# Optimization experiments

Measured on AMD Instinct MI355X. Metric: run time of the kernel, lower is better.

The kernel has to match this reference:

```python
import jax, jax.numpy as jnp
import numpy as np
from jax.scipy.special import gammaln, xlogy

B, S, C = 2, 2048, 1536
H, DK, DV = 8, 64, 192
F_REL = C // H  # 192 relative-position features


def positional_features_all(positions, feature_size, seq_length):
    # positions: [1, 2S-1] float32 (signed relative distances)
    n = feature_size // 6  # basis per class per sign
    ap = jnp.abs(positions)  # [1, 2S-1]
    Sf = float(seq_length)
    # exponential decay features
    max_range = float(np.log(Sf) / np.log(2.0))
    half_life = 2.0 ** jnp.linspace(3.0, max_range, n)  # min_half_life = 3.0
    feat_exp = jnp.exp(-jnp.log(2.0) / half_life * ap[..., None])
    # central mask features
    center_widths = 2.0 ** jnp.arange(1, n + 1, dtype=jnp.float32) - 1.0
    feat_cm = (center_widths > ap[..., None]).astype(jnp.float32)
    # gamma pdf features
    stddev = Sf / (2.0 * n)
    start_mean = Sf / n
    mean = jnp.linspace(start_mean, Sf, n)
    conc = (mean / stddev) ** 2
    rate = mean / (stddev ** 2)
    xg = ap[..., None]
    log_unnorm = xlogy(conc - 1.0, xg) - rate * xg
    log_norm = gammaln(conc) - conc * jnp.log(rate)
    prob = jnp.exp(log_unnorm - log_norm) + 1e-8
    feat_g = prob / jnp.max(prob, axis=1, keepdims=True)
    emb = jnp.concatenate([feat_exp, feat_cm, feat_g], axis=-1)  # [1, 2S-1, 3n]
    emb = jnp.concatenate([emb, jnp.sign(positions)[..., None] * emb], axis=-1)
    return emb  # [1, 2S-1, feature_size]


def relative_shift(x):
    # x: [B, H, T, 2T-1] -> [B, H, T, T] (Transformer-XL shift trick)
    b, h, t, _ = x.shape
    x = jnp.pad(x, ((0, 0), (0, 0), (0, 0), (1, 0)))  # [B,H,T,2T]
    x = x.reshape(b, h, 2 * t, t)[:, :, 1:, :]          # [B,H,2T-1,T]
    x = x.reshape(b, h, t, 2 * t - 1)[:, :, :, :t]      # [B,H,T,T]
    return x


def setup_inputs() -> dict:
    key = jax.random.key(0)
    ks = jax.random.split(key, 8)
    inp = {
        "x": jax.random.normal(ks[0], (B, S, C), dtype=jnp.float32),
        "mask": jax.random.randint(ks[1], (B, S), 0, 2, dtype=jnp.int32),
        "Wq": jax.random.normal(ks[2], (C, H * DK), dtype=jnp.float32) * 0.02,
        "Wk": jax.random.normal(ks[3], (C, H * DK), dtype=jnp.float32) * 0.02,
        "Wv": jax.random.normal(ks[4], (C, H * DV), dtype=jnp.float32) * 0.02,
        "Wr": jax.random.normal(ks[5], (F_REL, H * DK), dtype=jnp.float32) * 0.02,
        "r_w_bias": jax.random.normal(ks[6], (1, H, 1, DK), dtype=jnp.float32) * 0.02,
        "Wo": jax.random.normal(ks[7], (H * DV, H * DV), dtype=jnp.float32) * 0.02,
        "bo": jnp.zeros((H * DV,), dtype=jnp.float32),
    }
    return inp


def reference(x, mask, Wq, Wk, Wv, Wr, r_w_bias, Wo, bo):
    b, s, c = x.shape
    # projections -> [B, H, S, d]
    q = (x @ Wq).reshape(b, s, H, DK).transpose(0, 2, 1, 3) * (DK ** -0.5)
    k = (x @ Wk).reshape(b, s, H, DK).transpose(0, 2, 1, 3)
    v = (x @ Wv).reshape(b, s, H, DV).transpose(0, 2, 1, 3)
    # relative positional encodings for distances -S+1 .. S-1
    dist = jnp.arange(-s + 1, s, dtype=jnp.float32)[None, :]  # [1, 2S-1]
    pe = positional_features_all(dist, F_REL, s)               # [1, 2S-1, F_REL]
    r_k = (pe[0] @ Wr).reshape(2 * s - 1, H, DK).transpose(1, 0, 2)  # [H, 2S-1, DK]
    # content + position logits
    content_logits = jnp.einsum('bhqd,bhkd->bhqk', q, k)                   # [B,H,S,S]
    rel_logits = jnp.einsum('bhqd,hkd->bhqk', q + r_w_bias, r_k)           # [B,H,S,2S-1]
    logits = content_logits + relative_shift(rel_logits)
    logits = jnp.where(mask[:, None, None, :] == 0, -1e9, logits)
    weights = jax.nn.softmax(logits, axis=-1)
    out = jnp.einsum('bhqk,bhkd->bhqd', weights, v)  # [B,H,S,DV]
    out = out.transpose(0, 2, 1, 3).reshape(b, s, H * DV)
    return out @ Wo + bo
```

## Files before the change

### kernel.cpp

```cpp
#include <hip/hip_runtime.h>
#include <math.h>

#define SEQ 2048
#define CDIM 1536
#define HN 8
#define DVC 192
#define BN 2
#define NPOS 4095
#define HDK 512
#define HDV 1536
#define PSTR 72

typedef __attribute__((ext_vector_type(8))) _Float16 hf8v;
typedef __attribute__((ext_vector_type(4))) _Float16 hf4v;
typedef __attribute__((ext_vector_type(4))) float f4v;

static __device__ __forceinline__ f4v mfma16(hf8v a, hf8v b, f4v c) {
  return __builtin_amdgcn_mfma_f32_16x16x32_f16(a, b, c, 0, 0, 0);
}
static __device__ __forceinline__ void gl2lds16(const void* g, void* l) {
  __builtin_amdgcn_global_load_lds((const __attribute__((address_space(1))) unsigned int*)g,
                                   (__attribute__((address_space(3))) unsigned int*)l,
                                   16, 0, 0);
}
static __device__ __forceinline__ float rowmax16(float x) {
  x = fmaxf(x, __int_as_float(__builtin_amdgcn_update_dpp(0, __float_as_int(x), 0x128, 0xf, 0xf, true)));
  x = fmaxf(x, __int_as_float(__builtin_amdgcn_update_dpp(0, __float_as_int(x), 0x124, 0xf, 0xf, true)));
  x = fmaxf(x, __int_as_float(__builtin_amdgcn_update_dpp(0, __float_as_int(x), 0x122, 0xf, 0xf, true)));
  x = fmaxf(x, __int_as_float(__builtin_amdgcn_update_dpp(0, __float_as_int(x), 0x121, 0xf, 0xf, true)));
  return x;
}

#define CAST_B 6144
#define TWQ_B  768
#define TWK_B  768
#define TWV_B  2304
#define TWO_B  2304
#define TWR_B  96
#define PE_B   1536
#define TW_END (CAST_B + TWQ_B + TWK_B + TWV_B + TWO_B + TWR_B)
#define PREP_BLOCKS (TW_END + PE_B)

__device__ __forceinline__ void twc_tile(const float* __restrict__ W, _Float16* __restrict__ WT,
                                         int K, int N, int tile, float (*tls)[33], int tid) {
  int ntn = N >> 5;
  int nt = tile % ntn, kt = tile / ntn;
  int k0 = kt * 32, n0 = nt * 32;
  int tx = tid & 31, ty = tid >> 5;
#pragma unroll
  for (int p = 0; p < 4; p++) tls[ty + p * 8][tx] = W[(size_t)(k0 + ty + p * 8) * N + n0 + tx];
  __syncthreads();
#pragma unroll
  for (int p = 0; p < 4; p++) {
    int n = ty + p * 8;
    WT[(size_t)(n0 + n) * K + k0 + tx] = (_Float16)tls[tx][n];
  }
}

__global__ __launch_bounds__(256) void prep_kernel(
    const float* __restrict__ x, const float* __restrict__ Wq, const float* __restrict__ Wk,
    const float* __restrict__ Wv, const float* __restrict__ Wo, const float* __restrict__ Wr,
    _Float16* __restrict__ xb, _Float16* __restrict__ WTqkv, _Float16* __restrict__ WoT,
    _Float16* __restrict__ WrT, _Float16* __restrict__ pe_h) {
  __shared__ float tls[32][33];
  int blk = blockIdx.x, tid = threadIdx.x;
  if (blk < CAST_B) {
    int i = (blk * 256 + tid) * 4;
    float4 v = *(const float4*)(x + i);
    _Float16 o[4] = {(_Float16)v.x, (_Float16)v.y, (_Float16)v.z, (_Float16)v.w};
    *(unsigned long long*)(xb + i) = *(const unsigned long long*)o;
  } else if (blk < CAST_B + TWQ_B) {
    twc_tile(Wq, WTqkv + 0 * (size_t)CDIM, CDIM, HDK, blk - CAST_B, tls, tid);
  } else if (blk < CAST_B + TWQ_B + TWK_B) {
    twc_tile(Wk, WTqkv + 512 * (size_t)CDIM, CDIM, HDK, blk - (CAST_B + TWQ_B), tls, tid);
  } else if (blk < CAST_B + TWQ_B + TWK_B + TWV_B) {
    twc_tile(Wv, WTqkv + 1024 * (size_t)CDIM, CDIM, HDV, blk - (CAST_B + TWQ_B + TWK_B), tls, tid);
  } else if (blk < CAST_B + TWQ_B + TWK_B + TWV_B + TWO_B) {
    twc_tile(Wo, WoT, CDIM, HDV, blk - (CAST_B + TWQ_B + TWK_B + TWV_B), tls, tid);
  } else if (blk < TW_END) {
    twc_tile(Wr, WrT, 192, HDK, blk - (CAST_B + TWQ_B + TWK_B + TWV_B + TWO_B), tls, tid);
  } else {
    int idx = (blk - TW_END) * 256 + tid;
    int pos = idx / 96, f = idx - pos * 96;
    float val = 0.0f, sval = 0.0f;
    if (pos < NPOS) {
      float ap = fabsf((float)(pos - (SEQ - 1)));
      int j = f & 31, cls = f >> 5;
      if (cls == 0) {
        float hl = exp2f(3.0f + 8.0f * (float)j / 31.0f);
        val = exp2f(-ap / hl);
      } else if (cls == 1) {
        float cw = exp2f((float)(j + 1)) - 1.0f;
        val = (cw > ap) ? 1.0f : 0.0f;
      } else {
        float conc = 4.0f * (float)((j + 1) * (j + 1));
        float rate = (float)(j + 1) / 16.0f;
        float log_norm = lgammaf(conc) - conc * logf(rate);
        float pv = expf((conc - 1.0f) * logf(ap) - rate * ap - log_norm) + 1e-8f;
        float mode = (conc - 1.0f) / rate;
        float a0 = fminf(floorf(mode), 2047.0f);
        float a1 = fminf(a0 + 1.0f, 2047.0f);
        float p0 = expf((conc - 1.0f) * logf(a0) - rate * a0 - log_norm) + 1e-8f;
        float p1 = expf((conc - 1.0f) * logf(a1) - rate * a1 - log_norm) + 1e-8f;
        val = pv / fmaxf(p0, p1);
      }
      float sgn = (pos > SEQ - 1) ? 1.0f : ((pos < SEQ - 1) ? -1.0f : 0.0f);
      sval = sgn * val;
    }
    pe_h[pos * 192 + f] = (_Float16)val;
    pe_h[pos * 192 + 96 + f] = (_Float16)sval;
  }
}

__global__ __launch_bounds__(256, 3) void mfma_gemm_qkvrk(
    const _Float16* __restrict__ xb, const _Float16* __restrict__ WTqkv,
    const _Float16* __restrict__ pe_h, const _Float16* __restrict__ WrT,
    _Float16* __restrict__ qb, _Float16* __restrict__ kb, _Float16* __restrict__ vtb,
    _Float16* __restrict__ rkb) {
  __shared__ __align__(16) _Float16 As[128 * 64];
  __shared__ __align__(16) _Float16 Bs[128 * 64];
  const int tid = threadIdx.x;
  const int lane = tid & 63, l15 = lane & 15, quad = lane >> 4;
  const int wv = tid >> 6;
  const int wm = (wv & 1) * 64, wn = (wv >> 1) * 64;
  const bool isrk = blockIdx.x >= 640;
  const _Float16* A;
  const _Float16* B;
  int K, ntx, lin, cpx;
  if (!isrk) {
    A = xb; B = WTqkv; K = CDIM; ntx = 20; lin = blockIdx.x; cpx = 80;
  } else {
    A = pe_h; B = WrT; K = 192; ntx = 4; lin = blockIdx.x - 640; cpx = 16;
  }
  const int sw = (lin & 7) * cpx + (lin >> 3);
  const int row0 = (sw / ntx) * 128, col0 = (sw % ntx) * 128;
  f4v acc[4][4];
#pragma unroll
  for (int i = 0; i < 4; i++)
#pragma unroll
    for (int j = 0; j < 4; j++) acc[i][j] = (f4v)0.0f;

  for (int k0 = 0; k0 < K; k0 += 64) {
    __syncthreads();
#pragma unroll
    for (int p = 0; p < 4; p++) {
      int idx = tid + p * 256;
      int rr = idx >> 3, sc = idx & 7;
      int gc = (sc ^ (rr & 7)) << 3;
      gl2lds16(A + (size_t)(row0 + rr) * K + k0 + gc, As + idx * 8);
      gl2lds16(B + (size_t)(col0 + rr) * K + k0 + gc, Bs + idx * 8);
    }
    __syncthreads();
#pragma unroll
    for (int kc = 0; kc < 2; kc++) {
      hf8v af[4], bfr[4];
#pragma unroll
      for (int t = 0; t < 4; t++) {
        int lrA = wm + t * 16 + l15;
        int lrB = wn + t * 16 + l15;
        af[t]  = *(const hf8v*)(As + lrA * 64 + ((((kc << 2) | quad) ^ (lrA & 7)) << 3));
        bfr[t] = *(const hf8v*)(Bs + lrB * 64 + ((((kc << 2) | quad) ^ (lrB & 7)) << 3));
      }
#pragma unroll
      for (int mt = 0; mt < 4; mt++)
#pragma unroll
        for (int nt = 0; nt < 4; nt++)
          acc[mt][nt] = mfma16(af[mt], bfr[nt], acc[mt][nt]);
    }
  }
#pragma unroll
  for (int mt = 0; mt < 4; mt++)
#pragma unroll
    for (int reg = 0; reg < 4; reg++) {
      int r = row0 + wm + mt * 16 + quad * 4 + reg;
      int bb = r >> 11, ss = r & (SEQ - 1);
#pragma unroll
      for (int nt = 0; nt < 4; nt++) {
        int c = col0 + wn + nt * 16 + l15;
        float vv = acc[mt][nt][reg];
        if (!isrk) {
          if (c < 512) {
            qb[(size_t)r * HDK + c] = (_Float16)(vv * 0.125f);
          } else if (c < 1024) {
            int cc = c - 512, h = cc >> 6, d = cc & 63;
            kb[(((size_t)bb * HN + h) * SEQ + ss) * 64 + d] = (_Float16)vv;
          } else {
            int cc = c - 1024, h = cc / DVC, e = cc - h * DVC;
            int jp = (ss & ~63) | ((ss & 15) << 2) | ((ss >> 4) & 3);
            vtb[(((size_t)bb * HN + h) * DVC + e) * SEQ + jp] = (_Float16)vv;
          }
        } else {
          int h = c >> 6, d = c & 63;
          rkb[((size_t)h * 4096 + r) * 64 + d] = (_Float16)vv;
        }
      }
    }
}

__global__ __launch_bounds__(256, 3) void mfma_gemm_out(
    const _Float16* __restrict__ A, const _Float16* __restrict__ B,
    const float* __restrict__ bias, float* __restrict__ out) {
  __shared__ __align__(16) _Float16 As[64 * 64];
  __shared__ __align__(16) _Float16 Bs[128 * 64];
  const int K = CDIM, ntx = 12;
  const int tid = threadIdx.x;
  const int lane = tid & 63, l15 = lane & 15, quad = lane >> 4;
  const int wv = tid >> 6;
  const int wm = (wv & 1) * 32, wn = (wv >> 1) * 64;
  const int lin = blockIdx.x;
  const int cpx = gridDim.x >> 3;
  const int sw = (lin & 7) * cpx + (lin >> 3);
  const int row0 = (sw / ntx) * 64, col0 = (sw % ntx) * 128;
  f4v acc[2][4];
#pragma unroll
  for (int i = 0; i < 2; i++)
#pragma unroll
    for (int j = 0; j < 4; j++) acc[i][j] = (f4v)0.0f;

  for (int k0 = 0; k0 < K; k0 += 64) {
    __syncthreads();
#pragma unroll
    for (int p = 0; p < 2; p++) {
      int idx = tid + p * 256;
      int rr = idx >> 3, sc = idx & 7;
      int gc = (sc ^ (rr & 7)) << 3;
      gl2lds16(A + (size_t)(row0 + rr) * K + k0 + gc, As + idx * 8);
    }
#pragma unroll
    for (int p = 0; p < 4; p++) {
      int idx = tid + p * 256;
      int rr = idx >> 3, sc = idx & 7;
      int gc = (sc ^ (rr & 7)) << 3;
      gl2lds16(B + (size_t)(col0 + rr) * K + k0 + gc, Bs + idx * 8);
    }
    __syncthreads();
#pragma unroll
    for (int kc = 0; kc < 2; kc++) {
      hf8v af[2], bfr[4];
#pragma unroll
      for (int t = 0; t < 2; t++) {
        int lrA = wm + t * 16 + l15;
        af[t] = *(const hf8v*)(As + lrA * 64 + ((((kc << 2) | quad) ^ (lrA & 7)) << 3));
      }
#pragma unroll
      for (int t = 0; t < 4; t++) {
        int lrB = wn + t * 16 + l15;
        bfr[t] = *(const hf8v*)(Bs + lrB * 64 + ((((kc << 2) | quad) ^ (lrB & 7)) << 3));
      }
#pragma unroll
      for (int mt = 0; mt < 2; mt++)
#pragma unroll
        for (int nt = 0; nt < 4; nt++)
          acc[mt][nt] = mfma16(af[mt], bfr[nt], acc[mt][nt]);
    }
  }
#pragma unroll
  for (int mt = 0; mt < 2; mt++)
#pragma unroll
    for (int reg = 0; reg < 4; reg++) {
      int r = row0 + wm + mt * 16 + quad * 4 + reg;
#pragma unroll
      for (int nt = 0; nt < 4; nt++) {
        int c = col0 + wn + nt * 16 + l15;
        out[(size_t)r * HDV + c] = acc[mt][nt][reg] + bias[c];
      }
    }
}

template <bool SPLITKV>
__global__ __launch_bounds__(256, 2) void attn_mfma(
    const _Float16* __restrict__ qb, const _Float16* __restrict__ kb,
    const _Float16* __restrict__ vtb, const _Float16* __restrict__ rkb,
    const float* __restrict__ rwb, const int* __restrict__ mask,
    _Float16* __restrict__ attn_out, float* __restrict__ Opart, float* __restrict__ ml) {
  __shared__ __align__(16) _Float16 Vts[192 * 64];
  __shared__ __align__(16) _Float16 RKs[192 * 64];
  __shared__ __align__(16) _Float16 Kts[64 * 64];
  __shared__ __align__(16) _Float16 Pbs[128 * PSTR];

  const int lin = blockIdx.x;
  const int chunk = SPLITKV ? 64 : 32;
  const int swz = (lin & 7) * chunk + (lin >> 3);
  const int bx = swz & 15;
  const int by = swz >> 4;
  const int i0 = bx * 128;
  const int bh = SPLITKV ? (by & 15) : by;
  const int half = SPLITKV ? (by >> 4) : 0;
  const int b = bh >> 3, h = bh & 7;
  const int tid = threadIdx.x;
  const int wv = tid >> 6, lane = tid & 63;
  const int l15 = lane & 15, quad = lane >> 4;

  hf8v qf[2][2], qbf[2][2];
#pragma unroll
  for (int s = 0; s < 2; s++) {
    int qrow = i0 + wv * 32 + s * 16 + l15;
    const _Float16* qp = qb + (size_t)(b * SEQ + qrow) * HDK + h * 64;
#pragma unroll
    for (int kc = 0; kc < 2; kc++) {
      hf8v qv = *(const hf8v*)(qp + kc * 32 + quad * 8);
      qf[s][kc] = qv;
      hf8v t;
#pragma unroll
      for (int j = 0; j < 8; j++)
        t[j] = (_Float16)((float)qv[j] + rwb[h * 64 + kc * 32 + quad * 8 + j]);
      qbf[s][kc] = t;
    }
  }

  f4v Of[2][12];
#pragma unroll
  for (int s = 0; s < 2; s++)
#pragma unroll
    for (int se = 0; se < 12; se++) Of[s][se] = (f4v)0.0f;
  float m_i[2][4] = {{-INFINITY, -INFINITY, -INFINITY, -INFINITY},
                     {-INFINITY, -INFINITY, -INFINITY, -INFINITY}};
  float l_i[2][4] = {{0.f, 0.f, 0.f, 0.f}, {0.f, 0.f, 0.f, 0.f}};

  const int j0beg = SPLITKV ? half * (SEQ / 2) : 0;
  const int j0end = SPLITKV ? j0beg + SEQ / 2 : SEQ;

  for (int j0 = j0beg; j0 < j0end; j0 += 64) {
    __syncthreads();
    int mraw[4];
#pragma unroll
    for (int st = 0; st < 4; st++) mraw[st] = mask[b * SEQ + j0 + st * 16 + l15];
    {
      const int U0 = j0 - i0 + 1920;
#pragma unroll
      for (int r = 0; r < 2; r++) {
        int idx = tid + r * 256, row = idx >> 3, sc = idx & 7;
        gl2lds16(kb + ((size_t)bh * SEQ + j0 + row) * 64 + ((sc ^ (row & 7)) << 3), Kts + idx * 8);
      }
#pragma unroll
      for (int r = 0; r < 6; r++) {
        int idx = tid + r * 256, row = idx >> 3, sc = idx & 7;
        gl2lds16(rkb + ((size_t)h * 4096 + U0 + row) * 64 + ((sc ^ (row & 7)) << 3), RKs + idx * 8);
      }
#pragma unroll
      for (int r = 0; r < 6; r++) {
        int idx = tid + r * 256, row = idx >> 3, sc = idx & 7;
        gl2lds16(vtb + ((size_t)bh * DVC + row) * SEQ + j0 + ((sc ^ (row & 7)) << 3), Vts + idx * 8);
      }
    }
    asm volatile("s_waitcnt vmcnt(6)" ::: "memory");
    __builtin_amdgcn_s_barrier();
    __builtin_amdgcn_sched_barrier(0);
    float mv[4];
#pragma unroll
    for (int st = 0; st < 4; st++) mv[st] = mraw[st] ? 0.f : -1e9f;

#pragma unroll
    for (int s = 0; s < 2; s++) {
      __builtin_amdgcn_s_setprio(1);
      f4v Sf[4];
#pragma unroll
      for (int st = 0; st < 4; st++) {
        Sf[st] = (f4v)0.0f;
#pragma unroll
        for (int kc = 0; kc < 2; kc++) {
          int row = st * 16 + l15;
          hf8v kf = *(const hf8v*)(Kts + row * 64 + ((((kc << 2) | quad) ^ (row & 7)) << 3));
          Sf[st] = mfma16(qf[s][kc], kf, Sf[st]);
        }
      }
      f4v Rf[5];
      const int tb = 112 - 32 * wv - 16 * s;
#pragma unroll
      for (int u = 0; u < 5; u++) {
        Rf[u] = (f4v)0.0f;
#pragma unroll
        for (int kc = 0; kc < 2; kc++) {
          int row = tb + u * 16 + l15;
          hf8v rf = *(const hf8v*)(RKs + row * 64 + ((((kc << 2) | quad) ^ (row & 7)) << 3));
          Rf[u] = mfma16(qbf[s][kc], rf, Rf[u]);
        }
      }
      __builtin_amdgcn_s_setprio(0);
#pragma unroll
      for (int reg = 0; reg < 4; reg++) {
        int delta = l15 - (quad << 2) - reg + 15;
        int srcl = (quad << 4) | (delta & 15);
        float sh0 = __shfl(Rf[0][reg], srcl, 64);
        float sh1 = __shfl(Rf[1][reg], srcl, 64);
        float sh2 = __shfl(Rf[2][reg], srcl, 64);
        float sh3 = __shfl(Rf[3][reg], srcl, 64);
        float sh4 = __shfl(Rf[4][reg], srcl, 64);
        bool hib = delta >= 16;
        Sf[0][reg] += (hib ? sh1 : sh0) + mv[0];
        Sf[1][reg] += (hib ? sh2 : sh1) + mv[1];
        Sf[2][reg] += (hib ? sh3 : sh2) + mv[2];
        Sf[3][reg] += (hib ? sh4 : sh3) + mv[3];
      }
#pragma unroll
      for (int reg = 0; reg < 4; reg++) {
        float t = fmaxf(fmaxf(Sf[0][reg], Sf[1][reg]), fmaxf(Sf[2][reg], Sf[3][reg]));
        t = rowmax16(t);
        if (__any(t - m_i[s][reg] > 8.0f)) {
          float mn = fmaxf(m_i[s][reg], t);
          float alpha = __expf(m_i[s][reg] - mn);
          m_i[s][reg] = mn;
          l_i[s][reg] *= alpha;
#pragma unroll
          for (int se = 0; se < 12; se++) Of[s][se][reg] *= alpha;
        }
        float mcur = m_i[s][reg];
        hf4v pv;
        float rs = 0.f;
#pragma unroll
        for (int st = 0; st < 4; st++) {
          float p = __expf(Sf[st][reg] - mcur);
          rs += p;
          pv[st] = (_Float16)p;
        }
        l_i[s][reg] += rs;
        *(hf4v*)(Pbs + (size_t)(wv * 32 + s * 16 + quad * 4 + reg) * PSTR + l15 * 4) = pv;
      }
    }

    hf8v pa[2][2];
#pragma unroll
    for (int s = 0; s < 2; s++)
#pragma unroll
      for (int kc = 0; kc < 2; kc++)
        pa[s][kc] = *(const hf8v*)(Pbs + (size_t)(wv * 32 + s * 16 + l15) * PSTR +
                                   kc * 32 + quad * 8);
    asm volatile("s_waitcnt vmcnt(0)" ::: "memory");
    __builtin_amdgcn_s_barrier();
    __builtin_amdgcn_sched_barrier(0);
    __builtin_amdgcn_s_setprio(1);
#pragma unroll
    for (int se = 0; se < 12; se++) {
#pragma unroll
      for (int kc = 0; kc < 2; kc++) {
        int row = se * 16 + l15;
        hf8v vf = *(const hf8v*)(Vts + row * 64 + ((((kc << 2) | quad) ^ (row & 7)) << 3));
        Of[0][se] = mfma16(pa[0][kc], vf, Of[0][se]);
        Of[1][se] = mfma16(pa[1][kc], vf, Of[1][se]);
      }
    }
    __builtin_amdgcn_s_setprio(0);
  }

#pragma unroll
  for (int s = 0; s < 2; s++)
#pragma unroll
    for (int reg = 0; reg < 4; reg++) {
      float ls = l_i[s][reg];
      ls += __shfl_xor(ls, 1);
      ls += __shfl_xor(ls, 2);
      ls += __shfl_xor(ls, 4);
      ls += __shfl_xor(ls, 8);
      int row = i0 + wv * 32 + s * 16 + quad * 4 + reg;
      int rg = b * SEQ + row;
      if constexpr (SPLITKV) {
        float* Op = Opart + ((size_t)(half * 4096 + rg)) * HDV + h * DVC;
#pragma unroll
        for (int se = 0; se < 12; se++) Op[se * 16 + l15] = Of[s][se][reg];
        if (l15 == 0) {
          size_t mlb = (((size_t)half * 4096 + rg) * HN + h) * 2;
          ml[mlb] = m_i[s][reg];
          ml[mlb + 1] = ls;
        }
      } else {
        float inv = 1.0f / ls;
        size_t base2 = (size_t)rg * HDV + h * DVC;
#pragma unroll
        for (int se = 0; se < 12; se++)
          attn_out[base2 + se * 16 + l15] = (_Float16)(Of[s][se][reg] * inv);
      }
    }
}

__global__ __launch_bounds__(256) void combine_kernel(const float* __restrict__ Opart,
                                                      const float* __restrict__ ml,
                                                      _Float16* __restrict__ attn_out) {
  int i4 = blockIdx.x * 256 + threadIdx.x;
  int rg = i4 / 384, c4 = (i4 - rg * 384) * 4;
  int h = c4 / DVC;
  size_t mlb0 = ((size_t)rg * HN + h) * 2;
  size_t mlb1 = (((size_t)4096 + rg) * HN + h) * 2;
  float m0 = ml[mlb0], l0 = ml[mlb0 + 1];
  float m1 = ml[mlb1], l1 = ml[mlb1 + 1];
  float M = fmaxf(m0, m1);
  float w0 = __expf(m0 - M), w1 = __expf(m1 - M);
  float inv = 1.0f / (l0 * w0 + l1 * w1);
  float4 O0 = *(const float4*)(Opart + (size_t)rg * HDV + c4);
  float4 O1 = *(const float4*)(Opart + ((size_t)4096 + rg) * HDV + c4);
  _Float16 o[4] = {(_Float16)((O0.x * w0 + O1.x * w1) * inv),
                   (_Float16)((O0.y * w0 + O1.y * w1) * inv),
                   (_Float16)((O0.z * w0 + O1.z * w1) * inv),
                   (_Float16)((O0.w * w0 + O1.w * w1) * inv)};
  *(unsigned long long*)(attn_out + (size_t)rg * HDV + c4) = *(const unsigned long long*)o;
}

extern "C" void kernel_launch(void* const* d_in, const int* in_sizes, int n_in,
                              void* d_out, int out_size, void* d_ws, size_t ws_size,
                              hipStream_t stream) {
  const float* x    = (const float*)d_in[0];
  const int*   mask = (const int*)d_in[1];
  const float* Wq   = (const float*)d_in[2];
  const float* Wk   = (const float*)d_in[3];
  const float* Wv   = (const float*)d_in[4];
  const float* Wr   = (const float*)d_in[5];
  const float* rwb  = (const float*)d_in[6];
  const float* Wo   = (const float*)d_in[7];
  const float* bo   = (const float*)d_in[8];
  float* out = (float*)d_out;

  char* wsb = (char*)d_ws;
  size_t o = 0;
  auto al = [](size_t v) { return (v + 255) & ~(size_t)255; };
#define CARVE(ptr_t, name, bytes) ptr_t name = (ptr_t)(wsb + o); o = al(o + (bytes));
  CARVE(_Float16*, pe_h, (size_t)4096 * 192 * 2)
  CARVE(_Float16*, WrT, (size_t)HDK * 192 * 2)
  CARVE(_Float16*, xb, (size_t)BN * SEQ * CDIM * 2)
  CARVE(_Float16*, WTqkv, (size_t)2560 * CDIM * 2)
  CARVE(_Float16*, WoT, (size_t)HDV * CDIM * 2)
  CARVE(_Float16*, qb, (size_t)BN * SEQ * HDK * 2)
  CARVE(_Float16*, kb, (size_t)BN * SEQ * HDK * 2)
  CARVE(_Float16*, vtb, (size_t)BN * SEQ * HDV * 2)
  CARVE(_Float16*, rkb, (size_t)HN * 4096 * 64 * 2)
  _Float16* attnh = xb;
  CARVE(float*, Opart, (size_t)2 * 4096 * HDV * 4)
  CARVE(float*, ml, (size_t)2 * 4096 * HN * 2 * 4)
  bool dosplit = (o <= ws_size);

  prep_kernel<<<PREP_BLOCKS, 256, 0, stream>>>(x, Wq, Wk, Wv, Wo, Wr, xb, WTqkv, WoT, WrT,
                                               pe_h);
  mfma_gemm_qkvrk<<<768, 256, 0, stream>>>(xb, WTqkv, pe_h, WrT, qb, kb, vtb, rkb);
  if (dosplit) {
    attn_mfma<true><<<512, 256, 0, stream>>>(qb, kb, vtb, rkb, rwb, mask,
                                             attnh, Opart, ml);
    combine_kernel<<<4096 * 384 / 256, 256, 0, stream>>>(Opart, ml, attnh);
  } else {
    attn_mfma<false><<<256, 256, 0, stream>>>(qb, kb, vtb, rkb, rwb, mask,
                                              attnh, nullptr, nullptr);
  }
  mfma_gemm_out<<<768, 256, 0, stream>>>(attnh, WoT, bo, out);
}
```

Baseline: 300.7 us.

## Prefetch next K and RK tiles during PV MFMA phase of attention loop

Moves the first tile's loads ahead of the loop and issues the next iteration's K, RK and mask loads right after the P-tile barrier, so they overlap the P·V MFMA work on the current V tile. The V tile for the next step is loaded after the PV compute behind an extra barrier, so Vts is not overwritten while it is still being read. The intent is to hide global-to-LDS latency for K/RK behind compute, at the cost of an added barrier per iteration and tighter ordering assumptions about reuse of the single LDS buffers.

```diff
diff --git a/kernel.cpp b/kernel.cpp
--- a/kernel.cpp
+++ b/kernel.cpp
@@ -320,32 +320,34 @@
   const int j0beg = SPLITKV ? half * (SEQ / 2) : 0;
   const int j0end = SPLITKV ? j0beg + SEQ / 2 : SEQ;
 
-  for (int j0 = j0beg; j0 < j0end; j0 += 64) {
-    __syncthreads();
-    int mraw[4];
+  int mraw[4];
+  {
+    const int j0 = j0beg;
 #pragma unroll
     for (int st = 0; st < 4; st++) mraw[st] = mask[b * SEQ + j0 + st * 16 + l15];
-    {
-      const int U0 = j0 - i0 + 1920;
-#pragma unroll
-      for (int r = 0; r < 2; r++) {
-        int idx = tid + r * 256, row = idx >> 3, sc = idx & 7;
-        gl2lds16(kb + ((size_t)bh * SEQ + j0 + row) * 64 + ((sc ^ (row & 7)) << 3), Kts + idx * 8);
-      }
-#pragma unroll
-      for (int r = 0; r < 6; r++) {
-        int idx = tid + r * 256, row = idx >> 3, sc = idx & 7;
-        gl2lds16(rkb + ((size_t)h * 4096 + U0 + row) * 64 + ((sc ^ (row & 7)) << 3), RKs + idx * 8);
-      }
-#pragma unroll
-      for (int r = 0; r < 6; r++) {
-        int idx = tid + r * 256, row = idx >> 3, sc = idx & 7;
-        gl2lds16(vtb + ((size_t)bh * DVC + row) * SEQ + j0 + ((sc ^ (row & 7)) << 3), Vts + idx * 8);
-      }
+    const int U0 = j0 - i0 + 1920;
+#pragma unroll
+    for (int r = 0; r < 2; r++) {
+      int idx = tid + r * 256, row = idx >> 3, sc = idx & 7;
+      gl2lds16(kb + ((size_t)bh * SEQ + j0 + row) * 64 + ((sc ^ (row & 7)) << 3), Kts + idx * 8);
+    }
+#pragma unroll
+    for (int r = 0; r < 6; r++) {
+      int idx = tid + r * 256, row = idx >> 3, sc = idx & 7;
+      gl2lds16(rkb + ((size_t)h * 4096 + U0 + row) * 64 + ((sc ^ (row & 7)) << 3), RKs + idx * 8);
+    }
+#pragma unroll
+    for (int r = 0; r < 6; r++) {
+      int idx = tid + r * 256, row = idx >> 3, sc = idx & 7;
+      gl2lds16(vtb + ((size_t)bh * DVC + row) * SEQ + j0 + ((sc ^ (row & 7)) << 3), Vts + idx * 8);
     }
     asm volatile("s_waitcnt vmcnt(6)" ::: "memory");
     __builtin_amdgcn_s_barrier();
     __builtin_amdgcn_sched_barrier(0);
+  }
+
+  for (int j0 = j0beg; j0 < j0end; j0 += 64) {
+    const bool notlast = (j0 + 64 < j0end);
     float mv[4];
 #pragma unroll
     for (int st = 0; st < 4; st++) mv[st] = mraw[st] ? 0.f : -1e9f;
@@ -428,6 +430,24 @@
     asm volatile("s_waitcnt vmcnt(0)" ::: "memory");
     __builtin_amdgcn_s_barrier();
     __builtin_amdgcn_sched_barrier(0);
+
+    if (notlast) {
+      const int j1 = j0 + 64;
+#pragma unroll
+      for (int st = 0; st < 4; st++) mraw[st] = mask[b * SEQ + j1 + st * 16 + l15];
+      const int U1 = j1 - i0 + 1920;
+#pragma unroll
+      for (int r = 0; r < 2; r++) {
+        int idx = tid + r * 256, row = idx >> 3, sc = idx & 7;
+        gl2lds16(kb + ((size_t)bh * SEQ + j1 + row) * 64 + ((sc ^ (row & 7)) << 3), Kts + idx * 8);
+      }
+#pragma unroll
+      for (int r = 0; r < 6; r++) {
+        int idx = tid + r * 256, row = idx >> 3, sc = idx & 7;
+        gl2lds16(rkb + ((size_t)h * 4096 + U1 + row) * 64 + ((sc ^ (row & 7)) << 3), RKs + idx * 8);
+      }
+    }
+
     __builtin_amdgcn_s_setprio(1);
 #pragma unroll
     for (int se = 0; se < 12; se++) {
@@ -440,6 +460,20 @@
       }
     }
     __builtin_amdgcn_s_setprio(0);
+
+    if (notlast) {
+      const int j1 = j0 + 64;
+      __builtin_amdgcn_s_barrier();
+      __builtin_amdgcn_sched_barrier(0);
+#pragma unroll
+      for (int r = 0; r < 6; r++) {
+        int idx = tid + r * 256, row = idx >> 3, sc = idx & 7;
+        gl2lds16(vtb + ((size_t)bh * DVC + row) * SEQ + j1 + ((sc ^ (row & 7)) << 3), Vts + idx * 8);
+      }
+      asm volatile("s_waitcnt vmcnt(6)" ::: "memory");
+      __builtin_amdgcn_s_barrier();
+      __builtin_amdgcn_sched_barrier(0);
+    }
   }
 
 #pragma unroll
```

Result: slower. 335.1 us (+11.4%).
